# Performance work log

Hardware: AMD Instinct MI355X
Metric: run time of the kernel (lower is better)

The kernel has to match this reference:

```python
import jax, jax.numpy as jnp
import numpy as np


def setup_inputs() -> dict:
    key = jax.random.key(0)
    ks = jax.random.split(key, 6)
    B, Nu, Ni, D = 256, 512, 512, 64
    u_fea = jax.random.normal(ks[0], (B, Nu, D), dtype=jnp.float32)
    i_fea = jax.random.normal(ks[1], (B, Ni, D), dtype=jnp.float32)
    M = jax.random.normal(ks[2], (D, D), dtype=jnp.float32)
    # Linear weights, torch-style: y = x @ W.T + b (init scaled like torch default)
    lim = 1.0 / np.sqrt(D)
    Wu = jax.random.uniform(ks[3], (D, D), minval=-lim, maxval=lim, dtype=jnp.float32)
    Wi = jax.random.uniform(ks[4], (D, D), minval=-lim, maxval=lim, dtype=jnp.float32)
    bu = jnp.zeros((D,), dtype=jnp.float32)
    bi = jnp.zeros((D,), dtype=jnp.float32)
    return {"u_fea": u_fea, "i_fea": i_fea, "M": M, "Wu": Wu, "bu": bu, "Wi": Wi, "bi": bi}


def reference(u_fea, i_fea, M, Wu, bu, Wi, bi):
    # fc_u / fc_i: torch Linear is x @ W.T + b
    u = jnp.einsum('bud,ed->bue', u_fea, Wu) + bu   # [B, Nu, D]
    i = jnp.einsum('bid,ed->bie', i_fea, Wi) + bi   # [B, Ni, D]
    # Bilinear co-attention score S = u @ M @ i^T  -> [B, Nu, Ni]
    uM = jnp.einsum('bud,de->bue', u, M)
    S = jnp.einsum('bue,bie->bui', uM, i)
    # pooling == 'max'
    u_score = S.max(axis=2)   # [B, Nu]
    i_score = S.max(axis=1)   # [B, Ni]
    # gumbel == False -> plain softmax over the review axis
    p_u = jax.nn.softmax(u_score, axis=1)
    p_i = jax.nn.softmax(i_score, axis=1)
    return (p_u[:, :, None], p_i[:, :, None])
```

## Files before the change

kernel.cpp:

```cpp
#include <hip/hip_runtime.h>
#include <float.h>


#define NBATCH 256
#define NSEQ   512
#define DIM    64

typedef __attribute__((ext_vector_type(8))) short short8;
typedef __attribute__((ext_vector_type(4))) float f32x4;

#define MFMA16(a,b,c) __builtin_amdgcn_mfma_f32_16x16x32_bf16(a,b,c,0,0,0)

__device__ __forceinline__ void cvt2(float f, unsigned short &h, unsigned short &l) {
    unsigned u = __float_as_uint(f);
    unsigned hb = (u + 0x7FFFu + ((u >> 16) & 1u)) >> 16;
    h = (unsigned short)hb;
    float r = f - __uint_as_float(hb << 16);
    unsigned u2 = __float_as_uint(r);
    l = (unsigned short)((u2 + 0x7FFFu + ((u2 >> 16) & 1u)) >> 16);
}

__device__ __forceinline__ void cvt8(const f32x4 a, const f32x4 b, short8 &hi, short8 &lo) {
    unsigned short h, l;
    #pragma unroll
    for (int i = 0; i < 4; ++i) { cvt2(a[i], h, l); hi[i] = (short)h; lo[i] = (short)l; }
    #pragma unroll
    for (int i = 0; i < 4; ++i) { cvt2(b[i], h, l); hi[4+i] = (short)h; lo[4+i] = (short)l; }
}

__global__ __launch_bounds__(64) void coatt_prep1(
    const float* __restrict__ M, const float* __restrict__ Wi,
    const float* __restrict__ bi, float* __restrict__ ws)
{
    __shared__ float Ml[64];
    const int d = blockIdx.x, f = threadIdx.x;
    Ml[f] = M[d*64 + f];
    __syncthreads();
    float s = 0.f;
    #pragma unroll 8
    for (int e = 0; e < 64; ++e) s = fmaf(Ml[e], Wi[e*64 + f], s);
    ws[8448 + d*64 + f] = s;
    float p = Ml[f] * bi[f];
    #pragma unroll
    for (int off = 1; off < 64; off <<= 1) p += __shfl_xor(p, off, 64);
    if (f == 0) ws[12544 + d] = p;
}

__global__ __launch_bounds__(64) void coatt_prep2(
    const float* __restrict__ Wu, const float* __restrict__ bu,
    float* __restrict__ ws)
{
    __shared__ float col[64];
    const int c = blockIdx.x, f = threadIdx.x;
    const float* T = ws + 8448;
    col[f] = Wu[f*64 + c];
    __syncthreads();
    float s = 0.f;
    #pragma unroll 8
    for (int d = 0; d < 64; ++d) s = fmaf(col[d], T[d*64 + f], s);
    unsigned short* efh = (unsigned short*)(ws + 4352);
    unsigned short* efl = efh + 4096;
    unsigned short h, l;
    cvt2(s, h, l);
    const int ko = c >> 5, quad = (c >> 3) & 3, j = c & 7;
    const int ft = f >> 4, f15 = f & 15;
    const int p = ft*1024 + ko*512 + (quad*16 + f15)*8 + j;
    efh[p] = h; efl[p] = l;
    float pa = col[f] * ws[12544 + f];
    #pragma unroll
    for (int off = 1; off < 64; off <<= 1) pa += __shfl_xor(pa, off, 64);
    if (f == 0) ws[4096 + c] = pa;
    if (c == 0) {
        float sg = 0.f;
        #pragma unroll 8
        for (int d = 0; d < 64; ++d) sg = fmaf(bu[d], T[d*64 + f], sg);
        ws[4160 + f] = sg;
        float ps = bu[f] * ws[12544 + f];
        #pragma unroll
        for (int off = 1; off < 64; off <<= 1) ps += __shfl_xor(ps, off, 64);
        if (f == 0) ws[4224] = ps;
    }
}

#define LDS_BYTES 160832

__global__ __launch_bounds__(256) void coatt_main(
    const float* __restrict__ u_fea, const float* __restrict__ i_fea,
    const float* __restrict__ ws, float* __restrict__ out)
{
    extern __shared__ char sm[];
    unsigned short* YH = (unsigned short*)sm;
    unsigned short* YL = (unsigned short*)(sm + 65536);
    const int t    = threadIdx.x;
    const int lane = t & 63, w = t >> 6, quad = lane >> 4, l15 = lane & 15;
    float* Xs     = (float*)(sm + 131072) + w * (16*68);
    float* rl     = (float*)(sm + 148480);
    float* colp   = (float*)(sm + 150528);
    float* uscore = (float*)(sm + 158720);
    float* red    = (float*)(sm + 160768);

    const int b = blockIdx.x;
    const float* ub = u_fea + (size_t)b * NSEQ * DIM;
    const float* ib = i_fea + (size_t)b * NSEQ * DIM;

    const unsigned short* efh = (const unsigned short*)(ws + 4352);
    const unsigned short* efl = efh + 4096;
    short8 EH[4][2], EL[4][2];
    #pragma unroll
    for (int ft = 0; ft < 4; ++ft)
        #pragma unroll
        for (int ko = 0; ko < 2; ++ko) {
            EH[ft][ko] = *(const short8*)(efh + ((ft*2+ko)*64 + lane)*8);
            EL[ft][ko] = *(const short8*)(efl + ((ft*2+ko)*64 + lane)*8);
        }
    float gb[4];
    #pragma unroll
    for (int ft = 0; ft < 4; ++ft) gb[ft] = ws[4160 + ft*16 + l15];
    const float s0 = ws[4224];

    for (int i = t; i < 2048; i += 256) colp[i] = -FLT_MAX;

    #pragma unroll 4
    for (int it = 0; it < 16; ++it) {
        const int v = it*256 + t;
        const int m = v >> 3, kq = v & 7;
        const f32x4* gp = (const f32x4*)(ib + m*64 + kq*8);
        const f32x4 f0 = gp[0], f1 = gp[1];
        short8 sh, sl;
        cvt8(f0, f1, sh, sl);
        const int off = (m>>4)*1024 + (kq>>2)*512 + ((kq&3)*16 + (m&15))*8;
        *(short8*)(YH + off) = sh;
        *(short8*)(YL + off) = sl;
    }

    {
        const f32x4* av = (const f32x4*)(ws + 4096);
        for (int r = t; r < NSEQ; r += 256) {
            const f32x4* up = (const f32x4*)(ub + r*64);
            float s = s0;
            #pragma unroll
            for (int c4 = 0; c4 < 16; ++c4) {
                const f32x4 u4 = up[c4], a4 = av[c4];
                s = fmaf(u4[0],a4[0],s); s = fmaf(u4[1],a4[1],s);
                s = fmaf(u4[2],a4[2],s); s = fmaf(u4[3],a4[3],s);
            }
            rl[r] = s;
        }
    }
    __syncthreads();

    #pragma unroll
    for (int h = 0; h < 2; ++h) {
        const int base = h*256 + w*64;
        short8 XH[4][2], XL[4][2];
        f32x4 rv[4];
        #pragma unroll
        for (int g = 0; g < 4; ++g) {
            const float* up = ub + (size_t)(base + g*16 + l15)*64 + quad*8;
            const f32x4 u0 = *(const f32x4*)up;
            const f32x4 u1 = *(const f32x4*)(up+4);
            const f32x4 u2 = *(const f32x4*)(up+32);
            const f32x4 u3 = *(const f32x4*)(up+36);
            short8 UH0, UL0, UH1, UL1;
            cvt8(u0,u1,UH0,UL0); cvt8(u2,u3,UH1,UL1);
            #pragma unroll
            for (int ft = 0; ft < 4; ++ft) {
                f32x4 c = {0.f,0.f,0.f,0.f};
                c = MFMA16(UH0, EH[ft][0], c);
                c = MFMA16(UH1, EH[ft][1], c);
                c = MFMA16(UH0, EL[ft][0], c);
                c = MFMA16(UH1, EL[ft][1], c);
                c = MFMA16(UL0, EH[ft][0], c);
                c = MFMA16(UL1, EH[ft][1], c);
                #pragma unroll
                for (int rg = 0; rg < 4; ++rg)
                    Xs[(quad*4+rg)*68 + ft*16 + l15] = c[rg] + gb[ft];
            }
            const float* xp = Xs + l15*68 + quad*8;
            const f32x4 x0 = *(const f32x4*)xp;
            const f32x4 x1 = *(const f32x4*)(xp+4);
            const f32x4 x2 = *(const f32x4*)(xp+32);
            const f32x4 x3 = *(const f32x4*)(xp+36);
            cvt8(x0,x1,XH[g][0],XL[g][0]);
            cvt8(x2,x3,XH[g][1],XL[g][1]);
            rv[g] = *(const f32x4*)(rl + base + g*16 + quad*4);
        }
        f32x4 rm[4];
        #pragma unroll
        for (int g = 0; g < 4; ++g)
            rm[g] = (f32x4){-FLT_MAX,-FLT_MAX,-FLT_MAX,-FLT_MAX};
        for (int T = 0; T < 32; ++T) {
            const unsigned short* yh2 = YH + T*1024 + lane*8;
            const unsigned short* yl2 = YL + T*1024 + lane*8;
            const short8 BH0 = *(const short8*)(yh2);
            const short8 BH1 = *(const short8*)(yh2 + 512);
            const short8 BL0 = *(const short8*)(yl2);
            const short8 BL1 = *(const short8*)(yl2 + 512);
            float cm = -FLT_MAX;
            #pragma unroll
            for (int g = 0; g < 4; ++g) {
                f32x4 c = {0.f,0.f,0.f,0.f};
                c = MFMA16(XH[g][0], BH0, c);
                c = MFMA16(XH[g][1], BH1, c);
                c = MFMA16(XH[g][0], BL0, c);
                c = MFMA16(XH[g][1], BL1, c);
                c = MFMA16(XL[g][0], BH0, c);
                c = MFMA16(XL[g][1], BH1, c);
                #pragma unroll
                for (int rg = 0; rg < 4; ++rg) {
                    const float s = c[rg] + rv[g][rg];
                    rm[g][rg] = fmaxf(rm[g][rg], s);
                    cm = fmaxf(cm, s);
                }
            }
            cm = fmaxf(cm, __shfl_xor(cm, 16, 64));
            cm = fmaxf(cm, __shfl_xor(cm, 32, 64));
            if (lane < 16) {
                float* cp = colp + w*512 + T*16 + lane;
                *cp = fmaxf(*cp, cm);
            }
        }
        #pragma unroll
        for (int g = 0; g < 4; ++g)
            #pragma unroll
            for (int rg = 0; rg < 4; ++rg) {
                float v = rm[g][rg];
                v = fmaxf(v, __shfl_xor(v, 1, 64));
                v = fmaxf(v, __shfl_xor(v, 2, 64));
                v = fmaxf(v, __shfl_xor(v, 4, 64));
                v = fmaxf(v, __shfl_xor(v, 8, 64));
                if (l15 == 0) uscore[base + g*16 + quad*4 + rg] = v;
            }
    }
    __syncthreads();
    for (int c = t; c < NSEQ; c += 256) {
        const float v = fmaxf(fmaxf(colp[c], colp[512+c]),
                              fmaxf(colp[1024+c], colp[1536+c]));
        colp[c] = v;
    }
    __syncthreads();

    {
        const int wid = t >> 6;
        float v = fmaxf(uscore[t], uscore[t+256]);
        #pragma unroll
        for (int off = 1; off < 64; off <<= 1) v = fmaxf(v, __shfl_xor(v, off, 64));
        if (lane == 0) red[wid] = v;
        __syncthreads();
        const float m = fmaxf(fmaxf(red[0], red[1]), fmaxf(red[2], red[3]));
        const float e0 = __expf(uscore[t] - m);
        const float e1 = __expf(uscore[t+256] - m);
        float s = e0 + e1;
        #pragma unroll
        for (int off = 1; off < 64; off <<= 1) s += __shfl_xor(s, off, 64);
        if (lane == 0) red[4+wid] = s;
        __syncthreads();
        const float inv = 1.0f / (red[4]+red[5]+red[6]+red[7]);
        out[(size_t)b*NSEQ + t]       = e0 * inv;
        out[(size_t)b*NSEQ + t + 256] = e1 * inv;
    }
    __syncthreads();
    {
        const int wid = t >> 6;
        float v = fmaxf(colp[t], colp[t+256]);
        #pragma unroll
        for (int off = 1; off < 64; off <<= 1) v = fmaxf(v, __shfl_xor(v, off, 64));
        if (lane == 0) red[8+wid] = v;
        __syncthreads();
        const float m = fmaxf(fmaxf(red[8], red[9]), fmaxf(red[10], red[11]));
        const float e0 = __expf(colp[t] - m);
        const float e1 = __expf(colp[t+256] - m);
        float s = e0 + e1;
        #pragma unroll
        for (int off = 1; off < 64; off <<= 1) s += __shfl_xor(s, off, 64);
        if (lane == 0) red[12+wid] = s;
        __syncthreads();
        const float inv = 1.0f / (red[12]+red[13]+red[14]+red[15]);
        out[(size_t)NBATCH*NSEQ + (size_t)b*NSEQ + t]       = e0 * inv;
        out[(size_t)NBATCH*NSEQ + (size_t)b*NSEQ + t + 256] = e1 * inv;
    }
}

extern "C" void kernel_launch(void* const* d_in, const int* in_sizes, int n_in,
                              void* d_out, int out_size, void* d_ws, size_t ws_size,
                              hipStream_t stream) {
    const float* u_fea = (const float*)d_in[0];
    const float* i_fea = (const float*)d_in[1];
    const float* M     = (const float*)d_in[2];
    const float* Wu    = (const float*)d_in[3];
    const float* bu    = (const float*)d_in[4];
    const float* Wi    = (const float*)d_in[5];
    const float* bi    = (const float*)d_in[6];
    float* out = (float*)d_out;
    float* ws  = (float*)d_ws;

    coatt_prep1<<<64, 64, 0, stream>>>(M, Wi, bi, ws);
    coatt_prep2<<<64, 64, 0, stream>>>(Wu, bu, ws);
    coatt_main<<<NBATCH, 256, LDS_BYTES, stream>>>(u_fea, i_fea, ws, out);
}
```

Before: 153.1 us.

## Use 512 threads per block with one row chunk per wave and aliased LDS

The main kernel now launches 512 threads (8 waves), so each wave handles one 64-row chunk of u instead of two chunks in sequence. The X scratch buffer is shrunk and the column-max buffer is aliased onto the scratch region to cut LDS use, which needs an extra barrier before colp is initialised. Bias terms are folded into the MFMA accumulator initial values rather than added afterwards. The goal is more waves in flight per CU to hide MFMA and LDS latency, at the cost of more registers per block and an 8-way column-max reduction.

```diff
diff --git a/kernel.cpp b/kernel.cpp
--- a/kernel.cpp
+++ b/kernel.cpp
@@ -82,9 +82,9 @@
     }
 }
 
-#define LDS_BYTES 160832
-
-__global__ __launch_bounds__(256) void coatt_main(
+#define LDS_BYTES 151552
+
+__global__ __launch_bounds__(512, 2) void coatt_main(
     const float* __restrict__ u_fea, const float* __restrict__ i_fea,
     const float* __restrict__ ws, float* __restrict__ out)
 {
@@ -93,11 +93,11 @@
     unsigned short* YL = (unsigned short*)(sm + 65536);
     const int t    = threadIdx.x;
     const int lane = t & 63, w = t >> 6, quad = lane >> 4, l15 = lane & 15;
-    float* Xs     = (float*)(sm + 131072) + w * (16*68);
-    float* rl     = (float*)(sm + 148480);
-    float* colp   = (float*)(sm + 150528);
-    float* uscore = (float*)(sm + 158720);
-    float* red    = (float*)(sm + 160768);
+    float* Xsw    = (float*)(sm + 131072) + w * 576;
+    float* rl     = (float*)(sm + 149504);
+    float* colp   = (float*)(sm + 131072);
+    float* uscore = (float*)(sm + 147456);
+    float* red    = (float*)(sm + 149504);
 
     const int b = blockIdx.x;
     const float* ub = u_fea + (size_t)b * NSEQ * DIM;
@@ -118,11 +118,9 @@
     for (int ft = 0; ft < 4; ++ft) gb[ft] = ws[4160 + ft*16 + l15];
     const float s0 = ws[4224];
 
-    for (int i = t; i < 2048; i += 256) colp[i] = -FLT_MAX;
-
-    #pragma unroll 4
-    for (int it = 0; it < 16; ++it) {
-        const int v = it*256 + t;
+    #pragma unroll
+    for (int it = 0; it < 8; ++it) {
+        const int v = it*512 + t;
         const int m = v >> 3, kq = v & 7;
         const f32x4* gp = (const f32x4*)(ib + m*64 + kq*8);
         const f32x4 f0 = gp[0], f1 = gp[1];
@@ -135,37 +133,36 @@
 
     {
         const f32x4* av = (const f32x4*)(ws + 4096);
-        for (int r = t; r < NSEQ; r += 256) {
-            const f32x4* up = (const f32x4*)(ub + r*64);
-            float s = s0;
+        const f32x4* up = (const f32x4*)(ub + t*64);
+        float s = s0;
+        #pragma unroll
+        for (int c4 = 0; c4 < 16; ++c4) {
+            const f32x4 u4 = up[c4], a4 = av[c4];
+            s = fmaf(u4[0],a4[0],s); s = fmaf(u4[1],a4[1],s);
+            s = fmaf(u4[2],a4[2],s); s = fmaf(u4[3],a4[3],s);
+        }
+        rl[t] = s;
+    }
+    __syncthreads();
+
+    const int base = w*64;
+    short8 XH[4][2], XL[4][2];
+    f32x4 rv[4];
+    #pragma unroll
+    for (int g = 0; g < 4; ++g) {
+        const float* up = ub + (size_t)(base + g*16 + l15)*64 + quad*8;
+        const f32x4 u0 = *(const f32x4*)up;
+        const f32x4 u1 = *(const f32x4*)(up+4);
+        const f32x4 u2 = *(const f32x4*)(up+32);
+        const f32x4 u3 = *(const f32x4*)(up+36);
+        short8 UH0, UL0, UH1, UL1;
+        cvt8(u0,u1,UH0,UL0); cvt8(u2,u3,UH1,UL1);
+        #pragma unroll
+        for (int fp = 0; fp < 2; ++fp) {
             #pragma unroll
-            for (int c4 = 0; c4 < 16; ++c4) {
-                const f32x4 u4 = up[c4], a4 = av[c4];
-                s = fmaf(u4[0],a4[0],s); s = fmaf(u4[1],a4[1],s);
-                s = fmaf(u4[2],a4[2],s); s = fmaf(u4[3],a4[3],s);
-            }
-            rl[r] = s;
-        }
-    }
-    __syncthreads();
-
-    #pragma unroll
-    for (int h = 0; h < 2; ++h) {
-        const int base = h*256 + w*64;
-        short8 XH[4][2], XL[4][2];
-        f32x4 rv[4];
-        #pragma unroll
-        for (int g = 0; g < 4; ++g) {
-            const float* up = ub + (size_t)(base + g*16 + l15)*64 + quad*8;
-            const f32x4 u0 = *(const f32x4*)up;
-            const f32x4 u1 = *(const f32x4*)(up+4);
-            const f32x4 u2 = *(const f32x4*)(up+32);
-            const f32x4 u3 = *(const f32x4*)(up+36);
-            short8 UH0, UL0, UH1, UL1;
-            cvt8(u0,u1,UH0,UL0); cvt8(u2,u3,UH1,UL1);
-            #pragma unroll
-            for (int ft = 0; ft < 4; ++ft) {
-                f32x4 c = {0.f,0.f,0.f,0.f};
+            for (int fh = 0; fh < 2; ++fh) {
+                const int ft = fp*2 + fh;
+                f32x4 c = {gb[ft], gb[ft], gb[ft], gb[ft]};
                 c = MFMA16(UH0, EH[ft][0], c);
                 c = MFMA16(UH1, EH[ft][1], c);
                 c = MFMA16(UH0, EL[ft][0], c);
@@ -174,110 +171,118 @@
                 c = MFMA16(UL1, EH[ft][1], c);
                 #pragma unroll
                 for (int rg = 0; rg < 4; ++rg)
-                    Xs[(quad*4+rg)*68 + ft*16 + l15] = c[rg] + gb[ft];
+                    Xsw[(quad*4+rg)*36 + fh*16 + l15] = c[rg];
             }
-            const float* xp = Xs + l15*68 + quad*8;
-            const f32x4 x0 = *(const f32x4*)xp;
-            const f32x4 x1 = *(const f32x4*)(xp+4);
-            const f32x4 x2 = *(const f32x4*)(xp+32);
-            const f32x4 x3 = *(const f32x4*)(xp+36);
-            cvt8(x0,x1,XH[g][0],XL[g][0]);
-            cvt8(x2,x3,XH[g][1],XL[g][1]);
-            rv[g] = *(const f32x4*)(rl + base + g*16 + quad*4);
-        }
-        f32x4 rm[4];
-        #pragma unroll
-        for (int g = 0; g < 4; ++g)
-            rm[g] = (f32x4){-FLT_MAX,-FLT_MAX,-FLT_MAX,-FLT_MAX};
-        for (int T = 0; T < 32; ++T) {
-            const unsigned short* yh2 = YH + T*1024 + lane*8;
-            const unsigned short* yl2 = YL + T*1024 + lane*8;
-            const short8 BH0 = *(const short8*)(yh2);
-            const short8 BH1 = *(const short8*)(yh2 + 512);
-            const short8 BL0 = *(const short8*)(yl2);
-            const short8 BL1 = *(const short8*)(yl2 + 512);
-            float cm = -FLT_MAX;
-            #pragma unroll
-            for (int g = 0; g < 4; ++g) {
-                f32x4 c = {0.f,0.f,0.f,0.f};
-                c = MFMA16(XH[g][0], BH0, c);
-                c = MFMA16(XH[g][1], BH1, c);
-                c = MFMA16(XH[g][0], BL0, c);
-                c = MFMA16(XH[g][1], BL1, c);
-                c = MFMA16(XL[g][0], BH0, c);
-                c = MFMA16(XL[g][1], BH1, c);
-                #pragma unroll
-                for (int rg = 0; rg < 4; ++rg) {
-                    const float s = c[rg] + rv[g][rg];
-                    rm[g][rg] = fmaxf(rm[g][rg], s);
-                    cm = fmaxf(cm, s);
-                }
+            const float* xp = Xsw + l15*36 + quad*8;
+            f32x4 x0, x1;
+            {
+                float2 p0 = *(const float2*)(xp);
+                float2 p1 = *(const float2*)(xp+2);
+                float2 p2 = *(const float2*)(xp+4);
+                float2 p3 = *(const float2*)(xp+6);
+                x0 = (f32x4){p0.x, p0.y, p1.x, p1.y};
+                x1 = (f32x4){p2.x, p2.y, p3.x, p3.y};
             }
-            cm = fmaxf(cm, __shfl_xor(cm, 16, 64));
-            cm = fmaxf(cm, __shfl_xor(cm, 32, 64));
-            if (lane < 16) {
-                float* cp = colp + w*512 + T*16 + lane;
-                *cp = fmaxf(*cp, cm);
-            }
-        }
-        #pragma unroll
-        for (int g = 0; g < 4; ++g)
-            #pragma unroll
-            for (int rg = 0; rg < 4; ++rg) {
-                float v = rm[g][rg];
-                v = fmaxf(v, __shfl_xor(v, 1, 64));
-                v = fmaxf(v, __shfl_xor(v, 2, 64));
-                v = fmaxf(v, __shfl_xor(v, 4, 64));
-                v = fmaxf(v, __shfl_xor(v, 8, 64));
-                if (l15 == 0) uscore[base + g*16 + quad*4 + rg] = v;
-            }
-    }
-    __syncthreads();
-    for (int c = t; c < NSEQ; c += 256) {
-        const float v = fmaxf(fmaxf(colp[c], colp[512+c]),
-                              fmaxf(colp[1024+c], colp[1536+c]));
-        colp[c] = v;
-    }
+            cvt8(x0, x1, XH[g][fp], XL[g][fp]);
+        }
+        rv[g] = *(const f32x4*)(rl + base + g*16 + quad*4);
+    }
+    __syncthreads();
+    for (int i = t; i < 4096; i += 512) colp[i] = -FLT_MAX;
+    __syncthreads();
+
+    f32x4 rm[4];
+    #pragma unroll
+    for (int g = 0; g < 4; ++g)
+        rm[g] = (f32x4){-FLT_MAX,-FLT_MAX,-FLT_MAX,-FLT_MAX};
+    for (int T = 0; T < 32; ++T) {
+        const unsigned short* yh2 = YH + T*1024 + lane*8;
+        const unsigned short* yl2 = YL + T*1024 + lane*8;
+        const short8 BH0 = *(const short8*)(yh2);
+        const short8 BH1 = *(const short8*)(yh2 + 512);
+        const short8 BL0 = *(const short8*)(yl2);
+        const short8 BL1 = *(const short8*)(yl2 + 512);
+        float cg[4];
+        #pragma unroll
+        for (int g = 0; g < 4; ++g) {
+            f32x4 c = rv[g];
+            c = MFMA16(XH[g][0], BH0, c);
+            c = MFMA16(XH[g][1], BH1, c);
+            c = MFMA16(XH[g][0], BL0, c);
+            c = MFMA16(XH[g][1], BL1, c);
+            c = MFMA16(XL[g][0], BH0, c);
+            c = MFMA16(XL[g][1], BH1, c);
+            rm[g][0] = fmaxf(rm[g][0], c[0]);
+            rm[g][1] = fmaxf(rm[g][1], c[1]);
+            rm[g][2] = fmaxf(rm[g][2], c[2]);
+            rm[g][3] = fmaxf(rm[g][3], c[3]);
+            cg[g] = fmaxf(fmaxf(c[0], c[1]), fmaxf(c[2], c[3]));
+        }
+        float cm = fmaxf(fmaxf(cg[0], cg[1]), fmaxf(cg[2], cg[3]));
+        cm = fmaxf(cm, __shfl_xor(cm, 16, 64));
+        cm = fmaxf(cm, __shfl_xor(cm, 32, 64));
+        if (lane < 16) {
+            float* cp = colp + w*512 + T*16 + lane;
+            *cp = fmaxf(*cp, cm);
+        }
+    }
+    #pragma unroll
+    for (int g = 0; g < 4; ++g)
+        #pragma unroll
+        for (int rg = 0; rg < 4; ++rg) {
+            float v = rm[g][rg];
+            v = fmaxf(v, __shfl_xor(v, 1, 64));
+            v = fmaxf(v, __shfl_xor(v, 2, 64));
+            v = fmaxf(v, __shfl_xor(v, 4, 64));
+            v = fmaxf(v, __shfl_xor(v, 8, 64));
+            if (l15 == 0) uscore[base + g*16 + quad*4 + rg] = v;
+        }
     __syncthreads();
 
     {
-        const int wid = t >> 6;
-        float v = fmaxf(uscore[t], uscore[t+256]);
-        #pragma unroll
-        for (int off = 1; off < 64; off <<= 1) v = fmaxf(v, __shfl_xor(v, off, 64));
-        if (lane == 0) red[wid] = v;
+        float v = uscore[t];
+        float m = v;
+        #pragma unroll
+        for (int off = 1; off < 64; off <<= 1) m = fmaxf(m, __shfl_xor(m, off, 64));
+        if (lane == 0) red[w] = m;
         __syncthreads();
-        const float m = fmaxf(fmaxf(red[0], red[1]), fmaxf(red[2], red[3]));
-        const float e0 = __expf(uscore[t] - m);
-        const float e1 = __expf(uscore[t+256] - m);
-        float s = e0 + e1;
+        m = red[0];
+        #pragma unroll
+        for (int q = 1; q < 8; ++q) m = fmaxf(m, red[q]);
+        const float e = __expf(v - m);
+        float s = e;
         #pragma unroll
         for (int off = 1; off < 64; off <<= 1) s += __shfl_xor(s, off, 64);
-        if (lane == 0) red[4+wid] = s;
+        if (lane == 0) red[8+w] = s;
         __syncthreads();
-        const float inv = 1.0f / (red[4]+red[5]+red[6]+red[7]);
-        out[(size_t)b*NSEQ + t]       = e0 * inv;
-        out[(size_t)b*NSEQ + t + 256] = e1 * inv;
+        float sum = red[8];
+        #pragma unroll
+        for (int q = 1; q < 8; ++q) sum += red[8+q];
+        out[(size_t)b*NSEQ + t] = e * (1.0f / sum);
     }
     __syncthreads();
     {
-        const int wid = t >> 6;
-        float v = fmaxf(colp[t], colp[t+256]);
-        #pragma unroll
-        for (int off = 1; off < 64; off <<= 1) v = fmaxf(v, __shfl_xor(v, off, 64));
-        if (lane == 0) red[8+wid] = v;
+        float v = colp[t];
+        #pragma unroll
+        for (int s8 = 1; s8 < 8; ++s8) v = fmaxf(v, colp[s8*512 + t]);
+        float m = v;
+        #pragma unroll
+        for (int off = 1; off < 64; off <<= 1) m = fmaxf(m, __shfl_xor(m, off, 64));
+        if (lane == 0) red[w] = m;
         __syncthreads();
-        const float m = fmaxf(fmaxf(red[8], red[9]), fmaxf(red[10], red[11]));
-        const float e0 = __expf(colp[t] - m);
-        const float e1 = __expf(colp[t+256] - m);
-        float s = e0 + e1;
+        m = red[0];
+        #pragma unroll
+        for (int q = 1; q < 8; ++q) m = fmaxf(m, red[q]);
+        const float e = __expf(v - m);
+        float s = e;
         #pragma unroll
         for (int off = 1; off < 64; off <<= 1) s += __shfl_xor(s, off, 64);
-        if (lane == 0) red[12+wid] = s;
+        if (lane == 0) red[8+w] = s;
         __syncthreads();
-        const float inv = 1.0f / (red[12]+red[13]+red[14]+red[15]);
-        out[(size_t)NBATCH*NSEQ + (size_t)b*NSEQ + t]       = e0 * inv;
-        out[(size_t)NBATCH*NSEQ + (size_t)b*NSEQ + t + 256] = e1 * inv;
+        float sum = red[8];
+        #pragma unroll
+        for (int q = 1; q < 8; ++q) sum += red[8+q];
+        out[(size_t)NBATCH*NSEQ + (size_t)b*NSEQ + t] = e * (1.0f / sum);
     }
 }
 
@@ -296,5 +301,5 @@
 
     coatt_prep1<<<64, 64, 0, stream>>>(M, Wi, bi, ws);
     coatt_prep2<<<64, 64, 0, stream>>>(Wu, bu, ws);
-    coatt_main<<<NBATCH, 256, LDS_BYTES, stream>>>(u_fea, i_fea, ws, out);
-}
+    coatt_main<<<NBATCH, 512, LDS_BYTES, stream>>>(u_fea, i_fea, ws, out);
+}
```

After: 148.8 us. 2.8% less time.
